# Optimization experiments

Measured on AMD Instinct MI355X. Metric: run time of the kernel, lower is better.

The kernel has to match this reference:

```python
import jax, jax.numpy as jnp
import numpy as np
from jax import lax

B, T, K, HID, NCLS = 32, 2048, 17, 64, 10
DILATIONS = (1, 1, 2)
RESIDUAL = (False, True, True)
TK = 3  # temporal kernel
BN_EPS = 1e-5
LN_EPS = 1e-5

COCO_EDGES = [(0,1),(0,2),(1,3),(2,4),(5,6),(5,7),(7,9),(6,8),(8,10),(5,11),(6,12),(11,13),(13,15),(12,14),(14,16)]

def build_skeleton_adj(num_kpts=K):
    adj = np.eye(num_kpts, dtype=np.float32)
    for i, j in COCO_EDGES:
        adj[i, j] = 1.0
        adj[j, i] = 1.0
    adj = adj + np.eye(num_kpts, dtype=np.float32)
    deg = adj.sum(axis=1, keepdims=True)
    deg[deg == 0] = 1.0
    return adj / deg

def setup_inputs() -> dict:
    key = jax.random.key(0)
    ks = jax.random.split(key, 8)
    kpts = jax.random.normal(ks[0], (B, T, K, 3), dtype=jnp.float32)
    adj = jnp.asarray(build_skeleton_adj(K))
    gcn_w0 = jax.random.normal(ks[1], (3, HID), dtype=jnp.float32) * (1.0 / np.sqrt(3))
    gcn_w1 = jax.random.normal(ks[2], (HID, HID), dtype=jnp.float32) * (1.0 / np.sqrt(HID))
    gcn_w2 = jax.random.normal(ks[3], (HID, HID), dtype=jnp.float32) * (1.0 / np.sqrt(HID))
    tcn_w = jax.random.normal(ks[4], (3, HID, HID, TK, 1), dtype=jnp.float32) * (1.0 / np.sqrt(HID * TK))
    bn_scale = 1.0 + 0.1 * jax.random.normal(ks[5], (3, HID), dtype=jnp.float32)
    bn_bias = 0.1 * jax.random.normal(ks[6], (3, HID), dtype=jnp.float32)
    bn_mean = 0.1 * jax.random.normal(ks[7], (3, HID), dtype=jnp.float32)
    bn_var = 0.5 + jax.random.uniform(jax.random.fold_in(key, 7), (3, HID), dtype=jnp.float32)
    ln_scale = jnp.ones((HID,), dtype=jnp.float32)
    ln_bias = jnp.zeros((HID,), dtype=jnp.float32)
    fc_w = jax.random.normal(jax.random.fold_in(key, 8), (HID, NCLS), dtype=jnp.float32) * (1.0 / np.sqrt(HID))
    fc_b = jnp.zeros((NCLS,), dtype=jnp.float32)
    return dict(kpts=kpts, adj=adj, gcn_w0=gcn_w0, gcn_w1=gcn_w1, gcn_w2=gcn_w2,
                tcn_w=tcn_w, bn_scale=bn_scale, bn_bias=bn_bias, bn_mean=bn_mean,
                bn_var=bn_var, ln_scale=ln_scale, ln_bias=ln_bias, fc_w=fc_w, fc_b=fc_b)

def _stgn_block(x, adj, gw, tw, bs, bb, bm, bv, dilation, residual):
    # x: [B, C_in, T, K]
    y = jnp.einsum('bctk,kv->bctv', x, adj)          # graph conv over keypoints
    y = jnp.einsum('bitk,io->botk', y, gw)           # channel mixing (intended GCN weight)
    pad = (TK - 1) * dilation // 2
    y = lax.conv_general_dilated(y, tw, window_strides=(1, 1),
                                 padding=[(pad, pad), (0, 0)],
                                 rhs_dilation=(dilation, 1),
                                 dimension_numbers=('NCHW', 'OIHW', 'NCHW'))
    inv = (bs / jnp.sqrt(bv + BN_EPS))[None, :, None, None]
    y = y * inv + (bb - bs * bm / jnp.sqrt(bv + BN_EPS))[None, :, None, None]
    y = jax.nn.relu(y)
    if residual:
        y = y + x
    return y

def reference(kpts, adj, gcn_w0, gcn_w1, gcn_w2, tcn_w, bn_scale, bn_bias, bn_mean,
              bn_var, ln_scale, ln_bias, fc_w, fc_b):
    x = jnp.transpose(kpts, (0, 3, 1, 2))  # [B, 3, T, K]
    gws = (gcn_w0, gcn_w1, gcn_w2)
    for i in range(3):
        x = _stgn_block(x, adj, gws[i], tcn_w[i], bn_scale[i], bn_bias[i],
                        bn_mean[i], bn_var[i], DILATIONS[i], RESIDUAL[i])
    feat = x.mean(axis=(2, 3))  # [B, HID] temporal/spatial mean pool
    mu = feat.mean(axis=-1, keepdims=True)
    var = feat.var(axis=-1, keepdims=True)
    feat = (feat - mu) / jnp.sqrt(var + LN_EPS) * ln_scale + ln_bias
    return feat @ fc_w + fc_b  # [B, NCLS]
```

## Files before the change

### kernel.cpp

```cpp
#include <hip/hip_runtime.h>
#include <hip/hip_fp16.h>
#include <math.h>

#define T_DIM 2048
#define TP_DIM 2052
#define K_DIM 17
#define HID   64
#define B_DIM 32

typedef short s16x8 __attribute__((ext_vector_type(8)));
typedef unsigned u32x2 __attribute__((ext_vector_type(2)));
typedef float f32x4 __attribute__((ext_vector_type(4)));
typedef _Float16 f16x2 __attribute__((ext_vector_type(2)));

__device__ __forceinline__ unsigned pkh(float lo, float hi) {
    return __builtin_bit_cast(unsigned, __builtin_amdgcn_cvt_pkrtz(lo, hi));
}
__device__ __forceinline__ f16x2 u2h(unsigned v) {
    return __builtin_bit_cast(f16x2, v);
}
__device__ __forceinline__ unsigned h2u(f16x2 v) {
    return __builtin_bit_cast(unsigned, v);
}
__device__ __forceinline__ short f2h(float f) {
    _Float16 h = (_Float16)f;
    return __builtin_bit_cast(short, h);
}

static constexpr int NBR_PTR[18] = {0,3,6,9,11,13,17,21,24,27,29,31,34,37,40,43,45,47};
static constexpr int NBR_K[47] = {
    0,1,2,  0,1,3,  0,2,4,  1,3,  2,4,
    5,6,7,11,  5,6,8,12,  5,7,9,  6,8,10,  7,9,  8,10,
    5,11,13,  6,12,14,  11,13,15,  12,14,16,  13,15,  14,16 };
__device__ const int d_NBR_PTR[18] = {0,3,6,9,11,13,17,21,24,27,29,31,34,37,40,43,45,47};
__device__ const int d_NBR_K[47] = {
    0,1,2,  0,1,3,  0,2,4,  1,3,  2,4,
    5,6,7,11,  5,6,8,12,  5,7,9,  6,8,10,  7,9,  8,10,
    5,11,13,  6,12,14,  11,13,15,  12,14,16,  13,15,  14,16 };

__global__ void fold_weights_kernel(
    const float* __restrict__ gw0, const float* __restrict__ gw1,
    const float* __restrict__ gw2, const float* __restrict__ tcn,
    const float* __restrict__ bns, const float* __restrict__ bnb,
    const float* __restrict__ bnm, const float* __restrict__ bnv,
    short* __restrict__ effT0, short* __restrict__ effT12,
    float* __restrict__ bnc, short* __restrict__ y2, int cb)
{
    int tid = blockIdx.x * blockDim.x + threadIdx.x;
    int stride = gridDim.x * blockDim.x;
    for (int idx = tid; idx < 2048; idx += stride) {
        int o = idx >> 5, k = idx & 31, dt = k >> 3, cin = k & 7;
        float s = 0.f;
        if (dt < 3 && cin < 3)
            for (int m = 0; m < 64; m++)
                s += gw0[cin * 64 + m] * tcn[(o * 64 + m) * 3 + dt];
        effT0[idx] = f2h(s);
    }
    for (int idx = tid; idx < 24576; idx += stride) {
        int blk = idx / 12288;
        int r = idx - blk * 12288;
        int o = r / 192, k = r - o * 192, dt = k >> 6, c = k & 63;
        const float* gw = blk ? gw2 : gw1;
        const float* tw = tcn + (size_t)(blk + 1) * 64 * 64 * 3;
        float s = 0.f;
        for (int m = 0; m < 64; m++)
            s += gw[c * 64 + m] * tw[(o * 64 + m) * 3 + dt];
        effT12[idx] = f2h(s);
    }
    for (int i = tid; i < 192; i += stride) {
        float inv = bns[i] * rsqrtf(bnv[i] + 1e-5f);
        bnc[i] = inv;
        bnc[192 + i] = bnb[i] - bnm[i] * inv;
    }
    const int zn = cb * 4 * 1088;
    for (int z = tid; z < zn; z += stride) {
        int bb = z / (4 * 1088);
        int rr = z - bb * 4 * 1088;
        int pi = rr / 1088;
        int ci = rr - pi * 1088;
        int tp = (pi < 2) ? pi : (2048 + pi);
        y2[((size_t)(bb * TP_DIM + tp) * K_DIM) * 64 + ci] = 0;
    }
}

__global__ __launch_bounds__(256, 4) void stgcn_ab_kernel(
    const float* __restrict__ x, const float* __restrict__ adj,
    const short* __restrict__ effT0, const short* __restrict__ effT12,
    const float* __restrict__ bnc, short* __restrict__ y2)
{
    __shared__ unsigned adj_h[289];
    __shared__ __align__(16) float xtg[12 * 52];
    __shared__ __align__(16) short ybuf[170 * 72];

    const int tid = threadIdx.x;
    const int b = blockIdx.y;
    const int t0 = blockIdx.x * 8;
    const int lane = tid & 63, wave = tid >> 6;
    const int col = lane & 15, kgrp = lane >> 4;

    for (int i = tid; i < 289; i += 256) {
        float w = adj[i];
        adj_h[i] = pkh(w, w);
    }
    s16x8 af1 = *(const s16x8*)(effT0 + (wave * 16 + col) * 32 + kgrp * 8);
    s16x8 af2[6];
    #pragma unroll
    for (int kk = 0; kk < 6; kk++)
        af2[kk] = *(const s16x8*)(effT12 +
            (wave * 16 + col) * 192 + kk * 32 + kgrp * 8);

    for (int i = tid; i < 204; i += 256) {
        const int r = (i * 241) >> 12;
        const int j = i - r * 17;
        const int t = t0 - 2 + r;
        float a0 = 0.f, a1 = 0.f, a2 = 0.f;
        if (t >= 0 && t < T_DIM) {
            const float* xp = x + ((size_t)b * T_DIM + t) * 51;
            const int p0 = d_NBR_PTR[j], p1 = d_NBR_PTR[j + 1];
            for (int e = p0; e < p1; e++) {
                const int k = d_NBR_K[e];
                const float w = adj[k * 17 + j];
                a0 += w * xp[k * 3 + 0];
                a1 += w * xp[k * 3 + 1];
                a2 += w * xp[k * 3 + 2];
            }
        }
        float* op = &xtg[r * 52 + j * 3];
        op[0] = a0; op[1] = a1; op[2] = a2;
    }
    __syncthreads();

    {
        f32x4 inv4 = *(const f32x4*)&bnc[wave * 16 + kgrp * 4];
        f32x4 sh4  = *(const f32x4*)&bnc[192 + wave * 16 + kgrp * 4];
        for (int tile = 0; tile < 11; tile++) {
            const int r = tile * 16 + col;
            const int me = r < 170 ? r : 169;
            const int s = (me * 241) >> 12;
            const int j = me - s * 17;
            int4 bz = {0, 0, 0, 0};
            if (kgrp < 3) {
                const float* xp = &xtg[(s + kgrp) * 52 + j * 3];
                bz.x = (int)pkh(xp[0], xp[1]);
                bz.y = (int)pkh(xp[2], 0.f);
            }
            s16x8 bfr = __builtin_bit_cast(s16x8, bz);
            f32x4 acc = __builtin_amdgcn_mfma_f32_16x16x32_f16(
                af1, bfr, (f32x4){0.f, 0.f, 0.f, 0.f}, 0, 0, 0);
            const int t = t0 - 1 + s;
            const bool valid = (t >= 0) && (t < T_DIM);
            if (r < 170) {
                float v0 = valid ? fmaxf(acc[0] * inv4[0] + sh4[0], 0.f) : 0.f;
                float v1 = valid ? fmaxf(acc[1] * inv4[1] + sh4[1], 0.f) : 0.f;
                float v2 = valid ? fmaxf(acc[2] * inv4[2] + sh4[2], 0.f) : 0.f;
                float v3 = valid ? fmaxf(acc[3] * inv4[3] + sh4[3], 0.f) : 0.f;
                u32x2 st; st[0] = pkh(v0, v1); st[1] = pkh(v2, v3);
                *(u32x2*)&ybuf[r * 72 + wave * 16 + kgrp * 4] = st;
            }
        }
    }
    __syncthreads();

    f32x4 acc2[9];
    #pragma unroll
    for (int t2 = 0; t2 < 9; t2++) acc2[t2] = (f32x4){0.f, 0.f, 0.f, 0.f};
    #pragma unroll
    for (int kk = 0; kk < 6; kk++) {
        #pragma unroll
        for (int t2 = 0; t2 < 9; t2++) {
            const int r = t2 * 16 + col;
            const int me = r < 136 ? r : 135;
            s16x8 bfr = *(const s16x8*)&ybuf[
                (me + 17 * (kk >> 1)) * 72 + (kk & 1) * 32 + kgrp * 8];
            acc2[t2] = __builtin_amdgcn_mfma_f32_16x16x32_f16(
                af2[kk], bfr, acc2[t2], 0, 0, 0);
        }
    }
    unsigned rv[17];
    {
        const int tl = tid >> 5, o0 = (tid & 31) * 2;
        #pragma unroll
        for (int v = 0; v < 17; v++)
            rv[v] = *(const unsigned*)&ybuf[((tl + 1) * 17 + v) * 72 + o0];
    }
    __syncthreads();

    #pragma unroll
    for (int t2 = 0; t2 < 9; t2++) {
        const int r = t2 * 16 + col;
        if (r < 136) {
            u32x2 st;
            st[0] = pkh(acc2[t2][0], acc2[t2][1]);
            st[1] = pkh(acc2[t2][2], acc2[t2][3]);
            *(u32x2*)&ybuf[r * 72 + wave * 16 + kgrp * 4] = st;
        }
    }
    __syncthreads();

    {
        const int tl = tid >> 5, o0 = (tid & 31) * 2;
        const f16x2 inv2 = u2h(pkh(bnc[64 + o0], bnc[64 + o0 + 1]));
        const f16x2 sh2  = u2h(pkh(bnc[256 + o0], bnc[256 + o0 + 1]));
        const f16x2 zero = u2h(0u);
        f16x2 zk[17];
        #pragma unroll
        for (int k = 0; k < 17; k++)
            zk[k] = u2h(*(const unsigned*)&ybuf[(tl * 17 + k) * 72 + o0]);
        const size_t gout = ((size_t)b * TP_DIM + t0 + tl + 2) * K_DIM * 64;
        #pragma unroll
        for (int v = 0; v < 17; v++) {
            f16x2 g = zero;
            #pragma unroll
            for (int e = NBR_PTR[v]; e < NBR_PTR[v + 1]; e++) {
                int k = NBR_K[e];
                g = u2h(adj_h[k * 17 + v]) * zk[k] + g;
            }
            f16x2 val = __builtin_elementwise_max(g * inv2 + sh2, zero);
            val = val + u2h(rv[v]);
            *(unsigned*)&y2[gout + (size_t)v * 64 + o0] = h2u(val);
        }
    }
}

__global__ __launch_bounds__(256, 4) void stgcn_c_kernel(
    const short* __restrict__ y2, const float* __restrict__ adj,
    const short* __restrict__ effW3, const float* __restrict__ bnc,
    float* __restrict__ part, int b0)
{
    __shared__ unsigned adj_h[289];
    __shared__ __align__(16) short ybuf[204 * 72];

    float* pr = (float*)&ybuf[136 * 72];

    const int tid = threadIdx.x;
    const int b = blockIdx.y;
    const int t0 = blockIdx.x * 8;
    const int lane = tid & 63, wave = tid >> 6;
    const int col = lane & 15, kgrp = lane >> 4;

    for (int i = tid; i < 289; i += 256) {
        float w = adj[i];
        adj_h[i] = pkh(w, w);
    }
    s16x8 af3[6];
    #pragma unroll
    for (int kk = 0; kk < 6; kk++)
        af3[kk] = *(const s16x8*)(effW3 +
            (wave * 16 + col) * 192 + kk * 32 + kgrp * 8);

    {
        const short* base = y2 + ((size_t)b * TP_DIM + t0) * K_DIM * 64;
        for (int idx = tid; idx < 1632; idx += 256) {
            const int row = idx >> 3, c = idx & 7;
            *(s16x8*)&ybuf[row * 72 + c * 8] =
                *(const s16x8*)(base + (size_t)row * 64 + c * 8);
        }
    }
    __syncthreads();

    f32x4 acc3[9];
    #pragma unroll
    for (int t3 = 0; t3 < 9; t3++) acc3[t3] = (f32x4){0.f, 0.f, 0.f, 0.f};
    #pragma unroll
    for (int kk = 0; kk < 6; kk++) {
        #pragma unroll
        for (int t3 = 0; t3 < 9; t3++) {
            const int r = t3 * 16 + col;
            const int me = r < 136 ? r : 135;
            s16x8 bfr = *(const s16x8*)&ybuf[
                (me + 34 * (kk >> 1)) * 72 + (kk & 1) * 32 + kgrp * 8];
            acc3[t3] = __builtin_amdgcn_mfma_f32_16x16x32_f16(
                af3[kk], bfr, acc3[t3], 0, 0, 0);
        }
    }
    f16x2 rs = u2h(0u);
    {
        const int tl = tid >> 5, o0 = (tid & 31) * 2;
        #pragma unroll
        for (int v = 0; v < 17; v++)
            rs = rs + u2h(*(const unsigned*)&ybuf[((tl + 2) * 17 + v) * 72 + o0]);
    }
    __syncthreads();

    #pragma unroll
    for (int t3 = 0; t3 < 9; t3++) {
        const int r = t3 * 16 + col;
        if (r < 136) {
            u32x2 st;
            st[0] = pkh(acc3[t3][0], acc3[t3][1]);
            st[1] = pkh(acc3[t3][2], acc3[t3][3]);
            *(u32x2*)&ybuf[r * 72 + wave * 16 + kgrp * 4] = st;
        }
    }
    __syncthreads();

    {
        const int tl = tid >> 5, o0 = (tid & 31) * 2;
        const f16x2 inv2 = u2h(pkh(bnc[128 + o0], bnc[128 + o0 + 1]));
        const f16x2 sh2  = u2h(pkh(bnc[320 + o0], bnc[320 + o0 + 1]));
        const f16x2 zero = u2h(0u);
        f16x2 zk[17];
        #pragma unroll
        for (int k = 0; k < 17; k++)
            zk[k] = u2h(*(const unsigned*)&ybuf[(tl * 17 + k) * 72 + o0]);
        float ps0 = (float)rs[0], ps1 = (float)rs[1];
        #pragma unroll
        for (int v = 0; v < 17; v++) {
            f16x2 g = zero;
            #pragma unroll
            for (int e = NBR_PTR[v]; e < NBR_PTR[v + 1]; e++) {
                int k = NBR_K[e];
                g = u2h(adj_h[k * 17 + v]) * zk[k] + g;
            }
            f16x2 val = __builtin_elementwise_max(g * inv2 + sh2, zero);
            ps0 += (float)val[0];
            ps1 += (float)val[1];
        }
        *(float2*)&pr[tl * 64 + o0] = make_float2(ps0, ps1);
    }
    __syncthreads();
    if (tid < 64) {
        float s = 0.f;
        #pragma unroll
        for (int i = 0; i < 8; i++) s += pr[i * 64 + tid];
        part[((size_t)(b0 + b) * 256 + blockIdx.x) * 64 + tid] = s;
    }
}

__global__ __launch_bounds__(256) void finish_kernel(
    const float* __restrict__ part, const float* __restrict__ ln_s,
    const float* __restrict__ ln_b, const float* __restrict__ fc_w,
    const float* __restrict__ fc_b, float* __restrict__ out)
{
    __shared__ float red[4][64];
    __shared__ float ns[64];
    const int b = blockIdx.x;
    const int g = threadIdx.x >> 6, c = threadIdx.x & 63;
    float s = 0.f;
    for (int j = 0; j < 64; j++)
        s += part[((size_t)b * 256 + g * 64 + j) * 64 + c];
    red[g][c] = s;
    __syncthreads();
    if (threadIdx.x < 64) {
        float feat = (red[0][c] + red[1][c] + red[2][c] + red[3][c])
                   / (float)(T_DIM * K_DIM);
        float m = feat;
        #pragma unroll
        for (int off = 32; off > 0; off >>= 1) m += __shfl_down(m, off);
        m = __shfl(m, 0) / 64.f;
        float d = feat - m;
        float v = d * d;
        #pragma unroll
        for (int off = 32; off > 0; off >>= 1) v += __shfl_down(v, off);
        v = __shfl(v, 0) / 64.f;
        ns[c] = d * rsqrtf(v + 1e-5f) * ln_s[c] + ln_b[c];
    }
    __syncthreads();
    if (threadIdx.x < 10) {
        float o = fc_b[threadIdx.x];
        for (int i = 0; i < 64; i++) o += ns[i] * fc_w[i * 10 + threadIdx.x];
        out[b * 10 + threadIdx.x] = o;
    }
}

extern "C" void kernel_launch(void* const* d_in, const int* in_sizes, int n_in,
                              void* d_out, int out_size, void* d_ws, size_t ws_size,
                              hipStream_t stream)
{
    const float* kpts = (const float*)d_in[0];
    const float* adj  = (const float*)d_in[1];
    const float* gw0  = (const float*)d_in[2];
    const float* gw1  = (const float*)d_in[3];
    const float* gw2  = (const float*)d_in[4];
    const float* tcn  = (const float*)d_in[5];
    const float* bns  = (const float*)d_in[6];
    const float* bnb  = (const float*)d_in[7];
    const float* bnm  = (const float*)d_in[8];
    const float* bnv  = (const float*)d_in[9];
    const float* lns  = (const float*)d_in[10];
    const float* lnb  = (const float*)d_in[11];
    const float* fcw  = (const float*)d_in[12];
    const float* fcb  = (const float*)d_in[13];
    float* out = (float*)d_out;

    float* bnc  = (float*)d_ws;
    float* part = bnc + 384;
    short* effT0  = (short*)(part + (size_t)B_DIM * 256 * 64);
    short* effT12 = effT0 + 2048;
    short* y2     = effT12 + 24576;
    const size_t fixed_bytes = 384 * 4 + (size_t)B_DIM * 256 * 64 * 4
                             + 2048 * 2 + 24576 * 2;
    const size_t y2_per_b = (size_t)TP_DIM * K_DIM * 64 * 2;

    int cb = B_DIM;
    while (cb > 1 && fixed_bytes + (size_t)cb * y2_per_b > ws_size)
        cb >>= 1;

    fold_weights_kernel<<<64, 256, 0, stream>>>(gw0, gw1, gw2, tcn,
                                                bns, bnb, bnm, bnv,
                                                effT0, effT12, bnc, y2, cb);

    for (int b0 = 0; b0 < B_DIM; b0 += cb) {
        stgcn_ab_kernel<<<dim3(T_DIM / 8, cb), 256, 0, stream>>>(
            kpts + (size_t)b0 * T_DIM * K_DIM * 3, adj, effT0, effT12, bnc, y2);
        stgcn_c_kernel<<<dim3(T_DIM / 8, cb), 256, 0, stream>>>(
            y2, adj, effT12 + 12288, bnc, part, b0);
    }

    finish_kernel<<<B_DIM, 256, 0, stream>>>(part, lns, lnb, fcw, fcb, out);
}
```

Before: 227.3 us.

## Reorder block-0 graph conv after channel mixing and apply it in fp16 on LDS

The first block's graph convolution over keypoints used to run on the 3-channel input before the MFMA channel/temporal mix. Now the MFMA runs on raw inputs read straight from global memory. The adjacency aggregation is then applied afterwards on the 64-channel result in LDS with packed fp16 FMAs, fused with BN and ReLU. This removes the xtg staging buffer and one global gather loop, but it does more aggregation work (64 channels instead of 3) in reduced precision, plus an extra barrier pass.

```diff
diff --git a/kernel.cpp b/kernel.cpp
--- a/kernel.cpp
+++ b/kernel.cpp
@@ -89,7 +89,6 @@
     const float* __restrict__ bnc, short* __restrict__ y2)
 {
     __shared__ unsigned adj_h[289];
-    __shared__ __align__(16) float xtg[12 * 52];
     __shared__ __align__(16) short ybuf[170 * 72];
 
     const int tid = threadIdx.x;
@@ -109,54 +108,52 @@
         af2[kk] = *(const s16x8*)(effT12 +
             (wave * 16 + col) * 192 + kk * 32 + kgrp * 8);
 
-    for (int i = tid; i < 204; i += 256) {
-        const int r = (i * 241) >> 12;
-        const int j = i - r * 17;
-        const int t = t0 - 2 + r;
-        float a0 = 0.f, a1 = 0.f, a2 = 0.f;
-        if (t >= 0 && t < T_DIM) {
-            const float* xp = x + ((size_t)b * T_DIM + t) * 51;
-            const int p0 = d_NBR_PTR[j], p1 = d_NBR_PTR[j + 1];
-            for (int e = p0; e < p1; e++) {
-                const int k = d_NBR_K[e];
-                const float w = adj[k * 17 + j];
-                a0 += w * xp[k * 3 + 0];
-                a1 += w * xp[k * 3 + 1];
-                a2 += w * xp[k * 3 + 2];
+    for (int tile = 0; tile < 11; tile++) {
+        const int r = tile * 16 + col;
+        const int me = r < 170 ? r : 169;
+        const int s = (me * 241) >> 12;
+        const int k = me - s * 17;
+        const int tt = t0 - 2 + s + kgrp;
+        int4 bz = {0, 0, 0, 0};
+        if (kgrp < 3 && tt >= 0 && tt < T_DIM) {
+            const float* xp = x + ((size_t)b * T_DIM + tt) * 51 + k * 3;
+            bz.x = (int)pkh(xp[0], xp[1]);
+            bz.y = (int)pkh(xp[2], 0.f);
+        }
+        s16x8 bfr = __builtin_bit_cast(s16x8, bz);
+        f32x4 acc = __builtin_amdgcn_mfma_f32_16x16x32_f16(
+            af1, bfr, (f32x4){0.f, 0.f, 0.f, 0.f}, 0, 0, 0);
+        if (r < 170) {
+            u32x2 st;
+            st[0] = pkh(acc[0], acc[1]);
+            st[1] = pkh(acc[2], acc[3]);
+            *(u32x2*)&ybuf[r * 72 + wave * 16 + kgrp * 4] = st;
+        }
+    }
+    __syncthreads();
+
+    for (int i = tid; i < 320; i += 256) {
+        const int tl = i >> 5, o0 = (i & 31) * 2;
+        const f16x2 inv2 = u2h(pkh(bnc[o0], bnc[o0 + 1]));
+        const f16x2 sh2  = u2h(pkh(bnc[192 + o0], bnc[192 + o0 + 1]));
+        const f16x2 zero = u2h(0u);
+        f16x2 zk[17];
+        #pragma unroll
+        for (int k = 0; k < 17; k++)
+            zk[k] = u2h(*(const unsigned*)&ybuf[(tl * 17 + k) * 72 + o0]);
+        const int t = t0 - 1 + tl;
+        const bool valid = (t >= 0) && (t < T_DIM);
+        #pragma unroll
+        for (int v = 0; v < 17; v++) {
+            f16x2 g = zero;
+            #pragma unroll
+            for (int e = NBR_PTR[v]; e < NBR_PTR[v + 1]; e++) {
+                int k = NBR_K[e];
+                g = u2h(adj_h[k * 17 + v]) * zk[k] + g;
             }
-        }
-        float* op = &xtg[r * 52 + j * 3];
-        op[0] = a0; op[1] = a1; op[2] = a2;
-    }
-    __syncthreads();
-
-    {
-        f32x4 inv4 = *(const f32x4*)&bnc[wave * 16 + kgrp * 4];
-        f32x4 sh4  = *(const f32x4*)&bnc[192 + wave * 16 + kgrp * 4];
-        for (int tile = 0; tile < 11; tile++) {
-            const int r = tile * 16 + col;
-            const int me = r < 170 ? r : 169;
-            const int s = (me * 241) >> 12;
-            const int j = me - s * 17;
-            int4 bz = {0, 0, 0, 0};
-            if (kgrp < 3) {
-                const float* xp = &xtg[(s + kgrp) * 52 + j * 3];
-                bz.x = (int)pkh(xp[0], xp[1]);
-                bz.y = (int)pkh(xp[2], 0.f);
-            }
-            s16x8 bfr = __builtin_bit_cast(s16x8, bz);
-            f32x4 acc = __builtin_amdgcn_mfma_f32_16x16x32_f16(
-                af1, bfr, (f32x4){0.f, 0.f, 0.f, 0.f}, 0, 0, 0);
-            const int t = t0 - 1 + s;
-            const bool valid = (t >= 0) && (t < T_DIM);
-            if (r < 170) {
-                float v0 = valid ? fmaxf(acc[0] * inv4[0] + sh4[0], 0.f) : 0.f;
-                float v1 = valid ? fmaxf(acc[1] * inv4[1] + sh4[1], 0.f) : 0.f;
-                float v2 = valid ? fmaxf(acc[2] * inv4[2] + sh4[2], 0.f) : 0.f;
-                float v3 = valid ? fmaxf(acc[3] * inv4[3] + sh4[3], 0.f) : 0.f;
-                u32x2 st; st[0] = pkh(v0, v1); st[1] = pkh(v2, v3);
-                *(u32x2*)&ybuf[r * 72 + wave * 16 + kgrp * 4] = st;
-            }
+            f16x2 val = __builtin_elementwise_max(g * inv2 + sh2, zero);
+            *(unsigned*)&ybuf[(tl * 17 + v) * 72 + o0] =
+                valid ? h2u(val) : 0u;
         }
     }
     __syncthreads();
```

Result: slower. 243.6 us (+7.2%).
